# Kernel tuning notes

Measured on AMD Instinct MI355X. Metric: run time of the kernel, lower is better.

The kernel has to match this reference:

```python
import jax, jax.numpy as jnp
import numpy as np

B, T, IN_DIM = 16, 4096, 64
LAYER_DIM, OUT_DIM, NUM_LAYERS = 256, 64, 10


def _k1(w, b, x):
    # pointwise (kernel_size=1) conv: w [O,I], x [B,I,T] -> [B,O,T]
    return jnp.einsum('oi,bit->bot', w, x) + b[:, None]


def setup_inputs() -> dict:
    key = jax.random.key(0)
    ks = jax.random.split(key, 20)
    s = 0.05
    L = LAYER_DIM
    inp = {
        'x': jax.random.normal(ks[0], (B, T, IN_DIM), jnp.float32),
        'emb_w': jax.random.normal(ks[1], (L, IN_DIM), jnp.float32) * s,
        'emb_b': jax.random.normal(ks[2], (L,), jnp.float32) * s,
        'filt_w': jax.random.normal(ks[3], (NUM_LAYERS, L, L, 2), jnp.float32) * s,
        'filt_b': jax.random.normal(ks[4], (NUM_LAYERS, L), jnp.float32) * s,
        'gate_w': jax.random.normal(ks[5], (NUM_LAYERS, L, L, 2), jnp.float32) * s,
        'gate_b': jax.random.normal(ks[6], (NUM_LAYERS, L), jnp.float32) * s,
        'res_w': jax.random.normal(ks[7], (NUM_LAYERS, L, L), jnp.float32) * s,
        'res_b': jax.random.normal(ks[8], (NUM_LAYERS, L), jnp.float32) * s,
        'skip_w': jax.random.normal(ks[9], (NUM_LAYERS + 1, L, L), jnp.float32) * s,
        'skip_b': jax.random.normal(ks[10], (NUM_LAYERS + 1, L), jnp.float32) * s,
        'fin1_w': jax.random.normal(ks[11], (L, L), jnp.float32) * s,
        'fin1_b': jax.random.normal(ks[12], (L,), jnp.float32) * s,
        'fin2_w': jax.random.normal(ks[13], (L, L), jnp.float32) * s,
        'fin2_b': jax.random.normal(ks[14], (L,), jnp.float32) * s,
        'out_w': jax.random.normal(ks[15], (OUT_DIM, L), jnp.float32) * s,
        'out_b': jax.random.normal(ks[16], (OUT_DIM,), jnp.float32) * s,
    }
    return inp


def reference(x, emb_w, emb_b, filt_w, filt_b, gate_w, gate_b,
              res_w, res_b, skip_w, skip_b,
              fin1_w, fin1_b, fin2_w, fin2_b, out_w, out_b):
    # x: [B, T, IN] -> [B, IN, T]
    h = jnp.transpose(x, (0, 2, 1))
    h = jax.nn.relu(_k1(emb_w, emb_b, h))  # [B, L, T]
    final = _k1(skip_w[0], skip_b[0], h)
    Tlen = h.shape[-1]
    for i in range(NUM_LAYERS):
        dilate = 2 ** i
        # causal dilated conv, k=2: y[t] = W[...,1] @ h[t] + W[...,0] @ h[t-dilate]
        h_shift = jnp.pad(h, ((0, 0), (0, 0), (dilate, 0)))[:, :, :Tlen]
        def dconv(w, b):
            return (jnp.einsum('oi,bit->bot', w[:, :, 1], h) +
                    jnp.einsum('oi,bit->bot', w[:, :, 0], h_shift) + b[:, None])
        t_x = jnp.tanh(dconv(filt_w[i], filt_b[i]))
        s_x = jax.nn.sigmoid(dconv(gate_w[i], gate_b[i]))
        residual_x = _k1(res_w[i], res_b[i], h)
        gated = t_x * s_x
        skip_x = _k1(skip_w[i + 1], skip_b[i + 1], gated)
        h = skip_x + residual_x  # note: original code adds skip_x (not gated) to residual
        final = final + skip_x
    final = _k1(fin1_w, fin1_b, jax.nn.relu(final))
    final = _k1(fin2_w, fin2_b, jax.nn.relu(final))
    final = jnp.transpose(final, (0, 2, 1))  # [B, T, L]
    outputs = jnp.tanh(final @ out_w.T + out_b)  # apply_tanh=True
    return outputs
```

## Files before the change

kernel.cpp:

```cpp
#include <hip/hip_runtime.h>
#include <hip/hip_bf16.h>

#define Bn 16
#define Tn 4096
#define IN_DIM 64
#define L 256
#define NL 10
#define PADROWS 512
#define TP (Tn + PADROWS)
#define COLS 64

typedef __attribute__((ext_vector_type(8))) short short8;
typedef __attribute__((ext_vector_type(4))) float f32x4;
typedef unsigned short ushort_t;
typedef unsigned int uint_t;

__device__ inline ushort_t f2bf(float f) {
    uint_t u = __builtin_bit_cast(uint_t, f);
    u = u + 0x7fffu + ((u >> 16) & 1u);
    return (ushort_t)(u >> 16);
}

__device__ inline float fexp2f(float x) { return __builtin_amdgcn_exp2f(x); }
__device__ inline float frcpf(float x)  { return __builtin_amdgcn_rcpf(x); }
__device__ inline float tanh_fast(float x) {
    float e = fexp2f(x * 2.8853900817779268f);
    return 1.f - 2.f * frcpf(e + 1.f);
}
__device__ inline float sigm_fast(float x) {
    return frcpf(1.f + fexp2f(-1.4426950408889634f * x));
}

__device__ inline f32x4 mfma16(short8 a, short8 b, f32x4 c) {
    return __builtin_amdgcn_mfma_f32_16x16x32_bf16(a, b, c, 0, 0, 0);
}

__device__ inline void gld_lds16(const void* src, void* dst) {
    __builtin_amdgcn_global_load_lds(
        (const __attribute__((address_space(1))) void*)src,
        (__attribute__((address_space(3))) void*)dst, 16, 0, 0);
}

__device__ inline int xcd_swz(int bid) {
    return (bid & 7) * 128 + (bid >> 3);
}

__global__ void prep_kernel(
    const float* __restrict__ filt_w, const float* __restrict__ gate_w,
    const float* __restrict__ res_w,  const float* __restrict__ skip_w,
    const float* __restrict__ emb_w,  const float* __restrict__ fin1_w,
    const float* __restrict__ fin2_w, const float* __restrict__ out_w,
    ushort_t* __restrict__ Wfp, ushort_t* __restrict__ Wgp,
    ushort_t* __restrict__ Wrp, ushort_t* __restrict__ Wsp,
    ushort_t* __restrict__ Ws0, ushort_t* __restrict__ We,
    ushort_t* __restrict__ W1,  ushort_t* __restrict__ W2,
    ushort_t* __restrict__ Wo,
    ushort_t* __restrict__ h_a, ushort_t* __restrict__ h_b)
{
    const int stride = gridDim.x * blockDim.x;
    const int tid0 = blockIdx.x * blockDim.x + threadIdx.x;

    for (int idx = tid0; idx < NL * 16 * 1024 * 8; idx += stride) {
        int e  = idx & 7;
        int r  = (idx >> 3) & 15;
        int qq = (idx >> 7) & 3;
        int rg = (idx >> 9) & 15;
        int t  = (idx >> 13) & 15;
        int i  = idx >> 17;
        int row = rg * 16 + r;
        int k = t * 32 + qq * 8 + e;
        int tap = (k < 256) ? 1 : 0;
        int kk = k & 255;
        int src = ((i * 256 + row) * 256 + kk) * 2 + tap;
        Wfp[idx] = f2bf(filt_w[src]);
        Wgp[idx] = f2bf(gate_w[src]);
    }
    for (int idx = tid0; idx < NL * 8 * 1024 * 8; idx += stride) {
        int e  = idx & 7;
        int r  = (idx >> 3) & 15;
        int qq = (idx >> 7) & 3;
        int rg = (idx >> 9) & 15;
        int t  = (idx >> 13) & 7;
        int i  = idx >> 16;
        int row = rg * 16 + r;
        int k = t * 32 + qq * 8 + e;
        Wrp[idx] = f2bf(res_w[(i * 256 + row) * 256 + k]);
        Wsp[idx] = f2bf(skip_w[((i + 1) * 256 + row) * 256 + k]);
    }
    for (int idx = tid0; idx < L * L; idx += stride) {
        Ws0[idx] = f2bf(skip_w[idx]);
        W1[idx] = f2bf(fin1_w[idx]);
        W2[idx] = f2bf(fin2_w[idx]);
    }
    for (int idx = tid0; idx < L * IN_DIM; idx += stride) We[idx] = f2bf(emb_w[idx]);
    for (int idx = tid0; idx < 64 * L; idx += stride)     Wo[idx] = f2bf(out_w[idx]);
    for (int idx = tid0; idx < Bn * PADROWS * L; idx += stride) {
        int bb = idx >> 17;
        int r = idx & 131071;
        size_t off = (size_t)bb * TP * L + r;
        h_a[off] = 0;
        h_b[off] = 0;
    }
}

__global__ __launch_bounds__(512, 4) void emb_kernel(
    const float* __restrict__ x,
    const ushort_t* __restrict__ We, const float* __restrict__ eb,
    const ushort_t* __restrict__ Ws0, const float* __restrict__ sb0,
    ushort_t* __restrict__ h_out, float* __restrict__ fin)
{
    __shared__ __align__(16) char gt[32 * 1024];

    const int tid = threadIdx.x;
    const int w = tid >> 6;
    const int ln = tid & 63;
    const int q = ln >> 4;
    const int n16 = ln & 15;
    const int lid = xcd_swz(blockIdx.x);
    const int b = lid >> 6;
    const int t0 = (lid & 63) * COLS;
    const int row0 = w * 32;

    f32x4 acc[2][4];
    #pragma unroll
    for (int rt = 0; rt < 2; ++rt)
        #pragma unroll
        for (int ct = 0; ct < 4; ++ct) acc[rt][ct] = (f32x4){0.f, 0.f, 0.f, 0.f};

    #pragma unroll
    for (int ks = 0; ks < 2; ++ks) {
        const int k = ks * 32 + q * 8;
        short8 bfr[4];
        #pragma unroll
        for (int ct = 0; ct < 4; ++ct) {
            int c = ct * 16 + n16;
            const float* xp = x + ((size_t)(b * Tn + t0 + c)) * IN_DIM + k;
            f32x4 x0 = *(const f32x4*)xp;
            f32x4 x1 = *(const f32x4*)(xp + 4);
            short8 v;
            v[0] = (short)f2bf(x0[0]); v[1] = (short)f2bf(x0[1]);
            v[2] = (short)f2bf(x0[2]); v[3] = (short)f2bf(x0[3]);
            v[4] = (short)f2bf(x1[0]); v[5] = (short)f2bf(x1[1]);
            v[6] = (short)f2bf(x1[2]); v[7] = (short)f2bf(x1[3]);
            bfr[ct] = v;
        }
        #pragma unroll
        for (int rt = 0; rt < 2; ++rt) {
            int row = row0 + rt * 16 + n16;
            short8 a = *(const short8*)(We + row * IN_DIM + k);
            #pragma unroll
            for (int ct = 0; ct < 4; ++ct)
                acc[rt][ct] = mfma16(a, bfr[ct], acc[rt][ct]);
        }
    }

    ushort_t* hob = h_out + ((size_t)(b * TP + PADROWS + t0)) * L;
    #pragma unroll
    for (int rt = 0; rt < 2; ++rt) {
        int i0 = row0 + rt * 16 + q * 4;
        f32x4 eb4 = *(const f32x4*)(eb + i0);
        #pragma unroll
        for (int ct = 0; ct < 4; ++ct) {
            int c = ct * 16 + n16;
            f32x4 h0 = acc[rt][ct] + eb4;
            float v0 = fmaxf(h0[0], 0.f), v1 = fmaxf(h0[1], 0.f);
            float v2 = fmaxf(h0[2], 0.f), v3 = fmaxf(h0[3], 0.f);
            uint_t lo = (uint_t)f2bf(v0) | ((uint_t)f2bf(v1) << 16);
            uint_t hi = (uint_t)f2bf(v2) | ((uint_t)f2bf(v3) << 16);
            *(uint2*)(hob + (size_t)c * L + i0) = make_uint2(lo, hi);
            int byt = c * 512 + ((i0 * 2) ^ ((c & 7) << 4));
            *(uint2*)(gt + byt) = make_uint2(lo, hi);
        }
    }
    __syncthreads();

    f32x4 accs[2][4];
    #pragma unroll
    for (int rt = 0; rt < 2; ++rt)
        #pragma unroll
        for (int ct = 0; ct < 4; ++ct) accs[rt][ct] = (f32x4){0.f, 0.f, 0.f, 0.f};

    for (int ks = 0; ks < 8; ++ks) {
        const int k = ks * 32 + q * 8;
        short8 bg[4];
        #pragma unroll
        for (int ct = 0; ct < 4; ++ct) {
            int c = ct * 16 + n16;
            bg[ct] = *(const short8*)(gt + c * 512 + ((k * 2) ^ ((c & 7) << 4)));
        }
        #pragma unroll
        for (int rt = 0; rt < 2; ++rt) {
            int row = row0 + rt * 16 + n16;
            short8 a = *(const short8*)(Ws0 + row * L + k);
            #pragma unroll
            for (int ct = 0; ct < 4; ++ct)
                accs[rt][ct] = mfma16(a, bg[ct], accs[rt][ct]);
        }
    }
    float* fob = fin + ((size_t)(b * Tn + t0)) * L;
    #pragma unroll
    for (int rt = 0; rt < 2; ++rt) {
        int i0 = row0 + rt * 16 + q * 4;
        f32x4 sb4 = *(const f32x4*)(sb0 + i0);
        #pragma unroll
        for (int ct = 0; ct < 4; ++ct) {
            int c = ct * 16 + n16;
            *(f32x4*)(fob + (size_t)c * L + i0) = accs[rt][ct] + sb4;
        }
    }
}

__global__ __launch_bounds__(512, 4) void layer_kernel(
    const ushort_t* __restrict__ h_in, ushort_t* __restrict__ h_out,
    float* __restrict__ fin,
    const char* __restrict__ WfL, const char* __restrict__ WgL,
    const char* __restrict__ WrL, const char* __restrict__ WsL,
    const float* __restrict__ fb_, const float* __restrict__ gb_,
    const float* __restrict__ rb_, const float* __restrict__ sb_,
    int d)
{
    __shared__ __align__(16) char hh[64 * 1024];

    const int tid = threadIdx.x;
    const int w = tid >> 6;
    const int ln = tid & 63;
    const int q = ln >> 4;
    const int n16 = ln & 15;
    const int lid = xcd_swz(blockIdx.x);
    const int b = lid >> 6;
    const int t0 = (lid & 63) * COLS;

    const ushort_t* hbase = h_in + ((size_t)(b * TP + PADROWS + t0)) * L;
    #pragma unroll
    for (int it = 0; it < 8; ++it) {
        int c = it * 8 + w;
        int chunk = ln ^ (c & 7);
        int sh = (chunk >= 32) ? d : 0;
        const ushort_t* src = hbase + ((long)c - sh) * L + (chunk & 31) * 8;
        gld_lds16(src, hh + c * 1024);
    }
    __syncthreads();

    const char* pf = WfL + (w * 2) * 1024 + ln * 16;
    const char* pg = WgL + (w * 2) * 1024 + ln * 16;
    const char* ps = WsL + (w * 2) * 1024 + ln * 16;
    const char* pr = WrL + (w * 2) * 1024 + ln * 16;

    f32x4 accf[2][4], accg[2][4];
    #pragma unroll
    for (int rt = 0; rt < 2; ++rt)
        #pragma unroll
        for (int ct = 0; ct < 4; ++ct) {
            accf[rt][ct] = (f32x4){0.f, 0.f, 0.f, 0.f};
            accg[rt][ct] = (f32x4){0.f, 0.f, 0.f, 0.f};
        }

    short8 wf0 = *(const short8*)(pf);
    short8 wf1 = *(const short8*)(pf + 1024);
    short8 wg0 = *(const short8*)(pg);
    short8 wg1 = *(const short8*)(pg + 1024);
    for (int st = 0; st < 16; ++st) {
        const int nb = ((st < 15) ? st + 1 : 15) * 16384;
        short8 nf0 = *(const short8*)(pf + nb);
        short8 nf1 = *(const short8*)(pf + nb + 1024);
        short8 ng0 = *(const short8*)(pg + nb);
        short8 ng1 = *(const short8*)(pg + nb + 1024);
        const int kq2 = st * 64 + q * 16;
        #pragma unroll
        for (int ct = 0; ct < 4; ++ct) {
            int c = ct * 16 + n16;
            short8 bfr = *(const short8*)(hh + c * 1024 + (kq2 ^ ((c & 7) << 4)));
            accf[0][ct] = mfma16(wf0, bfr, accf[0][ct]);
            accf[1][ct] = mfma16(wf1, bfr, accf[1][ct]);
            accg[0][ct] = mfma16(wg0, bfr, accg[0][ct]);
            accg[1][ct] = mfma16(wg1, bfr, accg[1][ct]);
        }
        wf0 = nf0; wf1 = nf1; wg0 = ng0; wg1 = ng1;
    }
    __syncthreads();

    const int row0 = w * 32;
    #pragma unroll
    for (int rt = 0; rt < 2; ++rt) {
        int i0 = row0 + rt * 16 + q * 4;
        f32x4 fb4 = *(const f32x4*)(fb_ + i0);
        f32x4 gb4 = *(const f32x4*)(gb_ + i0);
        #pragma unroll
        for (int ct = 0; ct < 4; ++ct) {
            int c = ct * 16 + n16;
            uint_t pk[2];
            #pragma unroll
            for (int h2 = 0; h2 < 2; ++h2) {
                float v0 = tanh_fast(accf[rt][ct][h2 * 2] + fb4[h2 * 2]) *
                           sigm_fast(accg[rt][ct][h2 * 2] + gb4[h2 * 2]);
                float v1 = tanh_fast(accf[rt][ct][h2 * 2 + 1] + fb4[h2 * 2 + 1]) *
                           sigm_fast(accg[rt][ct][h2 * 2 + 1] + gb4[h2 * 2 + 1]);
                pk[h2] = (uint_t)f2bf(v0) | ((uint_t)f2bf(v1) << 16);
            }
            int byt = c * 1024 + ((512 + i0 * 2) ^ ((c & 7) << 4));
            *(uint2*)(hh + byt) = make_uint2(pk[0], pk[1]);
        }
    }
    __syncthreads();

    f32x4 accs[2][4], accr[2][4];
    #pragma unroll
    for (int rt = 0; rt < 2; ++rt)
        #pragma unroll
        for (int ct = 0; ct < 4; ++ct) {
            accs[rt][ct] = (f32x4){0.f, 0.f, 0.f, 0.f};
            accr[rt][ct] = (f32x4){0.f, 0.f, 0.f, 0.f};
        }

    short8 ws0 = *(const short8*)(ps);
    short8 ws1 = *(const short8*)(ps + 1024);
    short8 wr0 = *(const short8*)(pr);
    short8 wr1 = *(const short8*)(pr + 1024);
    for (int st = 0; st < 8; ++st) {
        const int nb = ((st < 7) ? st + 1 : 7) * 16384;
        short8 ns0 = *(const short8*)(ps + nb);
        short8 ns1 = *(const short8*)(ps + nb + 1024);
        short8 nr0 = *(const short8*)(pr + nb);
        short8 nr1 = *(const short8*)(pr + nb + 1024);
        const int kq2 = st * 64 + q * 16;
        #pragma unroll
        for (int ct = 0; ct < 4; ++ct) {
            int c = ct * 16 + n16;
            short8 bg = *(const short8*)(hh + c * 1024 +
                                         ((512 + kq2) ^ ((c & 7) << 4)));
            short8 bh = *(const short8*)(hh + c * 1024 + (kq2 ^ ((c & 7) << 4)));
            accs[0][ct] = mfma16(ws0, bg, accs[0][ct]);
            accs[1][ct] = mfma16(ws1, bg, accs[1][ct]);
            accr[0][ct] = mfma16(wr0, bh, accr[0][ct]);
            accr[1][ct] = mfma16(wr1, bh, accr[1][ct]);
        }
        ws0 = ns0; ws1 = ns1; wr0 = nr0; wr1 = nr1;
    }

    ushort_t* hob = h_out + ((size_t)(b * TP + PADROWS + t0)) * L;
    float* fob = fin + ((size_t)(b * Tn + t0)) * L;
    #pragma unroll
    for (int rt = 0; rt < 2; ++rt) {
        int i0 = row0 + rt * 16 + q * 4;
        f32x4 sb4 = *(const f32x4*)(sb_ + i0);
        f32x4 rb4 = *(const f32x4*)(rb_ + i0);
        #pragma unroll
        for (int ct = 0; ct < 4; ++ct) {
            int c = ct * 16 + n16;
            f32x4 sk = accs[rt][ct] + sb4;
            f32x4 hn = sk + accr[rt][ct] + rb4;
            uint_t lo = (uint_t)f2bf(hn[0]) | ((uint_t)f2bf(hn[1]) << 16);
            uint_t hi = (uint_t)f2bf(hn[2]) | ((uint_t)f2bf(hn[3]) << 16);
            *(uint2*)(hob + (size_t)c * L + i0) = make_uint2(lo, hi);
            f32x4* fp = (f32x4*)(fob + (size_t)c * L + i0);
            *fp = *fp + sk;
        }
    }
}

__global__ __launch_bounds__(512, 4) void final_kernel(
    const float* __restrict__ fin,
    const ushort_t* __restrict__ W1, const float* __restrict__ b1,
    const ushort_t* __restrict__ W2, const float* __restrict__ b2,
    const ushort_t* __restrict__ Wo, const float* __restrict__ ob,
    float* __restrict__ out)
{
    __shared__ __align__(16) char s1[32 * 1024];
    __shared__ __align__(16) char s2[32 * 1024];

    const int tid = threadIdx.x;
    const int w = tid >> 6;
    const int ln = tid & 63;
    const int q = ln >> 4;
    const int n16 = ln & 15;
    const int lid = xcd_swz(blockIdx.x);
    const int b = lid >> 6;
    const int t0 = (lid & 63) * COLS;
    const int row0 = w * 32;

    {
        int c = tid & 63;
        int kg = tid >> 6;
        const float* fp = fin + ((size_t)(b * Tn + t0 + c)) * L + kg * 32;
        #pragma unroll
        for (int j = 0; j < 8; ++j) {
            f32x4 v = *(const f32x4*)(fp + j * 4);
            uint_t lo = (uint_t)f2bf(fmaxf(v[0], 0.f)) | ((uint_t)f2bf(fmaxf(v[1], 0.f)) << 16);
            uint_t hi = (uint_t)f2bf(fmaxf(v[2], 0.f)) | ((uint_t)f2bf(fmaxf(v[3], 0.f)) << 16);
            int kk = kg * 32 + j * 4;
            *(uint2*)(s1 + c * 512 + ((kk * 2) ^ ((c & 7) << 4))) = make_uint2(lo, hi);
        }
    }
    __syncthreads();

    f32x4 acc[2][4];
    #pragma unroll
    for (int rt = 0; rt < 2; ++rt)
        #pragma unroll
        for (int ct = 0; ct < 4; ++ct) acc[rt][ct] = (f32x4){0.f, 0.f, 0.f, 0.f};
    for (int ks = 0; ks < 8; ++ks) {
        const int k = ks * 32 + q * 8;
        short8 bfr[4];
        #pragma unroll
        for (int ct = 0; ct < 4; ++ct) {
            int c = ct * 16 + n16;
            bfr[ct] = *(const short8*)(s1 + c * 512 + ((k * 2) ^ ((c & 7) << 4)));
        }
        #pragma unroll
        for (int rt = 0; rt < 2; ++rt) {
            int row = row0 + rt * 16 + n16;
            short8 a = *(const short8*)(W1 + row * L + k);
            #pragma unroll
            for (int ct = 0; ct < 4; ++ct) acc[rt][ct] = mfma16(a, bfr[ct], acc[rt][ct]);
        }
    }
    #pragma unroll
    for (int rt = 0; rt < 2; ++rt) {
        int i0 = row0 + rt * 16 + q * 4;
        f32x4 bb = *(const f32x4*)(b1 + i0);
        #pragma unroll
        for (int ct = 0; ct < 4; ++ct) {
            int c = ct * 16 + n16;
            f32x4 z = acc[rt][ct] + bb;
            uint_t lo = (uint_t)f2bf(fmaxf(z[0], 0.f)) | ((uint_t)f2bf(fmaxf(z[1], 0.f)) << 16);
            uint_t hi = (uint_t)f2bf(fmaxf(z[2], 0.f)) | ((uint_t)f2bf(fmaxf(z[3], 0.f)) << 16);
            *(uint2*)(s2 + c * 512 + ((i0 * 2) ^ ((c & 7) << 4))) = make_uint2(lo, hi);
        }
    }
    __syncthreads();

    #pragma unroll
    for (int rt = 0; rt < 2; ++rt)
        #pragma unroll
        for (int ct = 0; ct < 4; ++ct) acc[rt][ct] = (f32x4){0.f, 0.f, 0.f, 0.f};
    for (int ks = 0; ks < 8; ++ks) {
        const int k = ks * 32 + q * 8;
        short8 bfr[4];
        #pragma unroll
        for (int ct = 0; ct < 4; ++ct) {
            int c = ct * 16 + n16;
            bfr[ct] = *(const short8*)(s2 + c * 512 + ((k * 2) ^ ((c & 7) << 4)));
        }
        #pragma unroll
        for (int rt = 0; rt < 2; ++rt) {
            int row = row0 + rt * 16 + n16;
            short8 a = *(const short8*)(W2 + row * L + k);
            #pragma unroll
            for (int ct = 0; ct < 4; ++ct) acc[rt][ct] = mfma16(a, bfr[ct], acc[rt][ct]);
        }
    }
    #pragma unroll
    for (int rt = 0; rt < 2; ++rt) {
        int i0 = row0 + rt * 16 + q * 4;
        f32x4 bb = *(const f32x4*)(b2 + i0);
        #pragma unroll
        for (int ct = 0; ct < 4; ++ct) {
            int c = ct * 16 + n16;
            f32x4 z = acc[rt][ct] + bb;
            uint_t lo = (uint_t)f2bf(z[0]) | ((uint_t)f2bf(z[1]) << 16);
            uint_t hi = (uint_t)f2bf(z[2]) | ((uint_t)f2bf(z[3]) << 16);
            *(uint2*)(s1 + c * 512 + ((i0 * 2) ^ ((c & 7) << 4))) = make_uint2(lo, hi);
        }
    }
    __syncthreads();

    if (w < 4) {
        f32x4 acc3[4];
        #pragma unroll
        for (int ct = 0; ct < 4; ++ct) acc3[ct] = (f32x4){0.f, 0.f, 0.f, 0.f};
        for (int ks = 0; ks < 8; ++ks) {
            const int k = ks * 32 + q * 8;
            short8 bfr[4];
            #pragma unroll
            for (int ct = 0; ct < 4; ++ct) {
                int c = ct * 16 + n16;
                bfr[ct] = *(const short8*)(s1 + c * 512 + ((k * 2) ^ ((c & 7) << 4)));
            }
            short8 a = *(const short8*)(Wo + (w * 16 + n16) * L + k);
            #pragma unroll
            for (int ct = 0; ct < 4; ++ct) acc3[ct] = mfma16(a, bfr[ct], acc3[ct]);
        }
        int o0 = w * 16 + q * 4;
        f32x4 ob4 = *(const f32x4*)(ob + o0);
        float* obase = out + ((size_t)(b * Tn + t0)) * 64;
        #pragma unroll
        for (int ct = 0; ct < 4; ++ct) {
            int c = ct * 16 + n16;
            f32x4 v;
            #pragma unroll
            for (int j = 0; j < 4; ++j) v[j] = tanh_fast(acc3[ct][j] + ob4[j]);
            *(f32x4*)(obase + (size_t)c * 64 + o0) = v;
        }
    }
}

extern "C" void kernel_launch(void* const* d_in, const int* in_sizes, int n_in,
                              void* d_out, int out_size, void* d_ws, size_t ws_size,
                              hipStream_t stream)
{
    (void)in_sizes; (void)n_in; (void)out_size; (void)ws_size;
    const float* x      = (const float*)d_in[0];
    const float* emb_w  = (const float*)d_in[1];
    const float* emb_b  = (const float*)d_in[2];
    const float* filt_w = (const float*)d_in[3];
    const float* filt_b = (const float*)d_in[4];
    const float* gate_w = (const float*)d_in[5];
    const float* gate_b = (const float*)d_in[6];
    const float* res_w  = (const float*)d_in[7];
    const float* res_b  = (const float*)d_in[8];
    const float* skip_w = (const float*)d_in[9];
    const float* skip_b = (const float*)d_in[10];
    const float* fin1_w = (const float*)d_in[11];
    const float* fin1_b = (const float*)d_in[12];
    const float* fin2_w = (const float*)d_in[13];
    const float* fin2_b = (const float*)d_in[14];
    const float* out_w  = (const float*)d_in[15];
    const float* out_b  = (const float*)d_in[16];

    char* ws = (char*)d_ws;
    size_t off = 0;
    auto alloc = [&](size_t bytes) -> char* {
        char* p = ws + off;
        off += (bytes + 255) & ~(size_t)255;
        return p;
    };
    ushort_t* h_a = (ushort_t*)alloc((size_t)Bn * TP * L * 2);
    ushort_t* h_b = (ushort_t*)alloc((size_t)Bn * TP * L * 2);
    float*    fin = (float*)   alloc((size_t)Bn * Tn * L * 4);
    ushort_t* Wfp = (ushort_t*)alloc((size_t)NL * 16 * 1024 * 8 * 2);
    ushort_t* Wgp = (ushort_t*)alloc((size_t)NL * 16 * 1024 * 8 * 2);
    ushort_t* Wrp = (ushort_t*)alloc((size_t)NL * 8 * 1024 * 8 * 2);
    ushort_t* Wsp = (ushort_t*)alloc((size_t)NL * 8 * 1024 * 8 * 2);
    ushort_t* Ws0 = (ushort_t*)alloc((size_t)L * L * 2);
    ushort_t* We  = (ushort_t*)alloc((size_t)L * IN_DIM * 2);
    ushort_t* W1  = (ushort_t*)alloc((size_t)L * L * 2);
    ushort_t* W2  = (ushort_t*)alloc((size_t)L * L * 2);
    ushort_t* Wo  = (ushort_t*)alloc((size_t)64 * L * 2);

    prep_kernel<<<512, 256, 0, stream>>>(filt_w, gate_w, res_w, skip_w, emb_w,
        fin1_w, fin2_w, out_w, Wfp, Wgp, Wrp, Wsp, Ws0, We, W1, W2, Wo, h_a, h_b);

    emb_kernel<<<1024, 512, 0, stream>>>(x, We, emb_b, Ws0, skip_b, h_a, fin);

    ushort_t* hin = h_a;
    ushort_t* hout = h_b;
    for (int i = 0; i < NL; ++i) {
        layer_kernel<<<1024, 512, 0, stream>>>(hin, hout, fin,
            (const char*)Wfp + (size_t)i * 16 * 16384,
            (const char*)Wgp + (size_t)i * 16 * 16384,
            (const char*)Wrp + (size_t)i * 8 * 16384,
            (const char*)Wsp + (size_t)i * 8 * 16384,
            filt_b + i * L, gate_b + i * L, res_b + i * L, skip_b + (i + 1) * L,
            1 << i);
        ushort_t* t = hin; hin = hout; hout = t;
    }

    final_kernel<<<1024, 512, 0, stream>>>(fin, W1, fin1_b, W2, fin2_b,
        Wo, out_b, (float*)d_out);
}
```

Measured before the change: 1.027 ms.

## Store per-layer skip outputs as bf16 slabs and sum them in final kernel

Instead of each layer doing a read-modify-write on an fp32 skip accumulator (8 bytes of traffic per element per layer), each layer writes its skip output as bf16 into its own slab, and the final kernel reads all 11 slabs and sums them. Layer outputs are staged through LDS so the global stores are coalesced. A fallback path that coalesces the fp32 accumulation is kept for when the workspace is too small. The slab path needs much more workspace, and rounding skip values to bf16 before summing adds error.

```diff
diff --git a/kernel.cpp b/kernel.cpp
--- a/kernel.cpp
+++ b/kernel.cpp
@@ -19,6 +19,10 @@
     uint_t u = __builtin_bit_cast(uint_t, f);
     u = u + 0x7fffu + ((u >> 16) & 1u);
     return (ushort_t)(u >> 16);
+}
+__device__ inline float bf2f(ushort_t v) {
+    uint_t u = ((uint_t)v) << 16;
+    return __builtin_bit_cast(float, u);
 }
 
 __device__ inline float fexp2f(float x) { return __builtin_amdgcn_exp2f(x); }
@@ -103,11 +107,13 @@
     }
 }
 
+template<bool SLAB>
 __global__ __launch_bounds__(512, 4) void emb_kernel(
     const float* __restrict__ x,
     const ushort_t* __restrict__ We, const float* __restrict__ eb,
     const ushort_t* __restrict__ Ws0, const float* __restrict__ sb0,
-    ushort_t* __restrict__ h_out, float* __restrict__ fin)
+    ushort_t* __restrict__ h_out, ushort_t* __restrict__ skip0,
+    float* __restrict__ fin)
 {
     __shared__ __align__(16) char gt[32 * 1024];
 
@@ -197,7 +203,6 @@
                 accs[rt][ct] = mfma16(a, bg[ct], accs[rt][ct]);
         }
     }
-    float* fob = fin + ((size_t)(b * Tn + t0)) * L;
     #pragma unroll
     for (int rt = 0; rt < 2; ++rt) {
         int i0 = row0 + rt * 16 + q * 4;
@@ -205,14 +210,24 @@
         #pragma unroll
         for (int ct = 0; ct < 4; ++ct) {
             int c = ct * 16 + n16;
-            *(f32x4*)(fob + (size_t)c * L + i0) = accs[rt][ct] + sb4;
-        }
-    }
-}
-
+            f32x4 z = accs[rt][ct] + sb4;
+            if constexpr (SLAB) {
+                ushort_t* sob = skip0 + ((size_t)(b * Tn + t0)) * L;
+                uint_t lo = (uint_t)f2bf(z[0]) | ((uint_t)f2bf(z[1]) << 16);
+                uint_t hi = (uint_t)f2bf(z[2]) | ((uint_t)f2bf(z[3]) << 16);
+                *(uint2*)(sob + (size_t)c * L + i0) = make_uint2(lo, hi);
+            } else {
+                float* fob = fin + ((size_t)(b * Tn + t0)) * L;
+                *(f32x4*)(fob + (size_t)c * L + i0) = z;
+            }
+        }
+    }
+}
+
+template<bool SLAB>
 __global__ __launch_bounds__(512, 4) void layer_kernel(
     const ushort_t* __restrict__ h_in, ushort_t* __restrict__ h_out,
-    float* __restrict__ fin,
+    ushort_t* __restrict__ skip_out, float* __restrict__ fin,
     const char* __restrict__ WfL, const char* __restrict__ WgL,
     const char* __restrict__ WrL, const char* __restrict__ WsL,
     const float* __restrict__ fb_, const float* __restrict__ gb_,
@@ -297,7 +312,7 @@
                            sigm_fast(accg[rt][ct][h2 * 2 + 1] + gb4[h2 * 2 + 1]);
                 pk[h2] = (uint_t)f2bf(v0) | ((uint_t)f2bf(v1) << 16);
             }
-            int byt = c * 1024 + ((512 + i0 * 2) ^ ((c & 7) << 4));
+            int byt = c * 1024 + 512 + ((i0 * 2) ^ ((c & 7) << 4));
             *(uint2*)(hh + byt) = make_uint2(pk[0], pk[1]);
         }
     }
@@ -326,8 +341,8 @@
         #pragma unroll
         for (int ct = 0; ct < 4; ++ct) {
             int c = ct * 16 + n16;
-            short8 bg = *(const short8*)(hh + c * 1024 +
-                                         ((512 + kq2) ^ ((c & 7) << 4)));
+            short8 bg = *(const short8*)(hh + c * 1024 + 512 +
+                                         (kq2 ^ ((c & 7) << 4)));
             short8 bh = *(const short8*)(hh + c * 1024 + (kq2 ^ ((c & 7) << 4)));
             accs[0][ct] = mfma16(ws0, bg, accs[0][ct]);
             accs[1][ct] = mfma16(ws1, bg, accs[1][ct]);
@@ -336,9 +351,8 @@
         }
         ws0 = ns0; ws1 = ns1; wr0 = nr0; wr1 = nr1;
     }
-
-    ushort_t* hob = h_out + ((size_t)(b * TP + PADROWS + t0)) * L;
-    float* fob = fin + ((size_t)(b * Tn + t0)) * L;
+    __syncthreads();
+
     #pragma unroll
     for (int rt = 0; rt < 2; ++rt) {
         int i0 = row0 + rt * 16 + q * 4;
@@ -349,16 +363,44 @@
             int c = ct * 16 + n16;
             f32x4 sk = accs[rt][ct] + sb4;
             f32x4 hn = sk + accr[rt][ct] + rb4;
-            uint_t lo = (uint_t)f2bf(hn[0]) | ((uint_t)f2bf(hn[1]) << 16);
-            uint_t hi = (uint_t)f2bf(hn[2]) | ((uint_t)f2bf(hn[3]) << 16);
-            *(uint2*)(hob + (size_t)c * L + i0) = make_uint2(lo, hi);
-            f32x4* fp = (f32x4*)(fob + (size_t)c * L + i0);
-            *fp = *fp + sk;
-        }
-    }
-}
-
+            uint_t hlo = (uint_t)f2bf(hn[0]) | ((uint_t)f2bf(hn[1]) << 16);
+            uint_t hhi = (uint_t)f2bf(hn[2]) | ((uint_t)f2bf(hn[3]) << 16);
+            uint_t slo = (uint_t)f2bf(sk[0]) | ((uint_t)f2bf(sk[1]) << 16);
+            uint_t shi = (uint_t)f2bf(sk[2]) | ((uint_t)f2bf(sk[3]) << 16);
+            int sw = (i0 * 2) ^ ((c & 7) << 4);
+            *(uint2*)(hh + c * 1024 + sw) = make_uint2(hlo, hhi);
+            *(uint2*)(hh + c * 1024 + 512 + sw) = make_uint2(slo, shi);
+        }
+    }
+    __syncthreads();
+
+    ushort_t* hob = h_out + ((size_t)(b * TP + PADROWS + t0)) * L;
+    #pragma unroll
+    for (int it = 0; it < 8; ++it) {
+        int c = it * 8 + w;
+        short8 v = *(const short8*)(hh + c * 1024 + ((ln * 16) ^ ((c & 7) << 4)));
+        if constexpr (SLAB) {
+            ushort_t* sob = skip_out + ((size_t)(b * Tn + t0)) * L;
+            if (ln < 32) *(short8*)(hob + (size_t)c * L + ln * 8) = v;
+            else         *(short8*)(sob + (size_t)c * L + (ln - 32) * 8) = v;
+        } else {
+            if (ln < 32) *(short8*)(hob + (size_t)c * L + ln * 8) = v;
+            uint2 skb = *(const uint2*)(hh + c * 1024 + 512 +
+                                        ((ln * 8) ^ ((c & 7) << 4)));
+            float* fp = fin + ((size_t)(b * Tn + t0 + c)) * L + ln * 4;
+            f32x4 f = *(const f32x4*)fp;
+            f[0] += bf2f((ushort_t)(skb.x & 0xffff));
+            f[1] += bf2f((ushort_t)(skb.x >> 16));
+            f[2] += bf2f((ushort_t)(skb.y & 0xffff));
+            f[3] += bf2f((ushort_t)(skb.y >> 16));
+            *(f32x4*)fp = f;
+        }
+    }
+}
+
+template<bool SLAB>
 __global__ __launch_bounds__(512, 4) void final_kernel(
+    const ushort_t* __restrict__ skipbase, size_t slab,
     const float* __restrict__ fin,
     const ushort_t* __restrict__ W1, const float* __restrict__ b1,
     const ushort_t* __restrict__ W2, const float* __restrict__ b2,
@@ -378,7 +420,35 @@
     const int t0 = (lid & 63) * COLS;
     const int row0 = w * 32;
 
-    {
+    if constexpr (SLAB) {
+        const int c = tid >> 3;
+        const int j0 = tid & 7;
+        const size_t rowoff = ((size_t)(b * Tn + t0 + c)) * L;
+        float acc[4][8];
+        #pragma unroll
+        for (int jj = 0; jj < 4; ++jj)
+            #pragma unroll
+            for (int e = 0; e < 8; ++e) acc[jj][e] = 0.f;
+        for (int l = 0; l < NL + 1; ++l) {
+            const ushort_t* sp = skipbase + (size_t)l * slab + rowoff;
+            #pragma unroll
+            for (int jj = 0; jj < 4; ++jj) {
+                short8 v = *(const short8*)(sp + j0 * 8 + jj * 64);
+                #pragma unroll
+                for (int e = 0; e < 8; ++e)
+                    acc[jj][e] += bf2f((ushort_t)v[e]);
+            }
+        }
+        #pragma unroll
+        for (int jj = 0; jj < 4; ++jj) {
+            short8 v;
+            #pragma unroll
+            for (int e = 0; e < 8; ++e)
+                v[e] = (short)f2bf(fmaxf(acc[jj][e], 0.f));
+            int j = j0 + jj * 8;
+            *(short8*)(s1 + c * 512 + ((j * 16) ^ ((c & 7) << 4))) = v;
+        }
+    } else {
         int c = tid & 63;
         int kg = tid >> 6;
         const float* fp = fin + ((size_t)(b * Tn + t0 + c)) * L + kg * 32;
@@ -498,7 +568,7 @@
                               void* d_out, int out_size, void* d_ws, size_t ws_size,
                               hipStream_t stream)
 {
-    (void)in_sizes; (void)n_in; (void)out_size; (void)ws_size;
+    (void)in_sizes; (void)n_in; (void)out_size;
     const float* x      = (const float*)d_in[0];
     const float* emb_w  = (const float*)d_in[1];
     const float* emb_b  = (const float*)d_in[2];
@@ -517,6 +587,17 @@
     const float* out_w  = (const float*)d_in[15];
     const float* out_b  = (const float*)d_in[16];
 
+    const size_t SLAB = (size_t)Bn * Tn * L;
+    const size_t sz_h     = (size_t)Bn * TP * L * 2;
+    const size_t sz_slabs = (size_t)(NL + 1) * SLAB * 2;
+    const size_t sz_fin   = (size_t)Bn * Tn * L * 4;
+    const size_t sz_wfg   = (size_t)NL * 16 * 1024 * 8 * 2;
+    const size_t sz_wrs   = (size_t)NL * 8 * 1024 * 8 * 2;
+    const size_t sz_small = 3 * (size_t)L * L * 2 + (size_t)L * IN_DIM * 2 +
+                            (size_t)64 * L * 2 + 4096;
+    const size_t reqA = 2 * sz_h + sz_slabs + 2 * sz_wfg + 2 * sz_wrs + sz_small;
+    const bool useSlab = (ws_size >= reqA);
+
     char* ws = (char*)d_ws;
     size_t off = 0;
     auto alloc = [&](size_t bytes) -> char* {
@@ -524,13 +605,16 @@
         off += (bytes + 255) & ~(size_t)255;
         return p;
     };
-    ushort_t* h_a = (ushort_t*)alloc((size_t)Bn * TP * L * 2);
-    ushort_t* h_b = (ushort_t*)alloc((size_t)Bn * TP * L * 2);
-    float*    fin = (float*)   alloc((size_t)Bn * Tn * L * 4);
-    ushort_t* Wfp = (ushort_t*)alloc((size_t)NL * 16 * 1024 * 8 * 2);
-    ushort_t* Wgp = (ushort_t*)alloc((size_t)NL * 16 * 1024 * 8 * 2);
-    ushort_t* Wrp = (ushort_t*)alloc((size_t)NL * 8 * 1024 * 8 * 2);
-    ushort_t* Wsp = (ushort_t*)alloc((size_t)NL * 8 * 1024 * 8 * 2);
+    ushort_t* h_a   = (ushort_t*)alloc(sz_h);
+    ushort_t* h_b   = (ushort_t*)alloc(sz_h);
+    ushort_t* skipb = nullptr;
+    float*    fin   = nullptr;
+    if (useSlab) skipb = (ushort_t*)alloc(sz_slabs);
+    else         fin   = (float*)alloc(sz_fin);
+    ushort_t* Wfp = (ushort_t*)alloc(sz_wfg);
+    ushort_t* Wgp = (ushort_t*)alloc(sz_wfg);
+    ushort_t* Wrp = (ushort_t*)alloc(sz_wrs);
+    ushort_t* Wsp = (ushort_t*)alloc(sz_wrs);
     ushort_t* Ws0 = (ushort_t*)alloc((size_t)L * L * 2);
     ushort_t* We  = (ushort_t*)alloc((size_t)L * IN_DIM * 2);
     ushort_t* W1  = (ushort_t*)alloc((size_t)L * L * 2);
@@ -540,21 +624,41 @@
     prep_kernel<<<512, 256, 0, stream>>>(filt_w, gate_w, res_w, skip_w, emb_w,
         fin1_w, fin2_w, out_w, Wfp, Wgp, Wrp, Wsp, Ws0, We, W1, W2, Wo, h_a, h_b);
 
-    emb_kernel<<<1024, 512, 0, stream>>>(x, We, emb_b, Ws0, skip_b, h_a, fin);
-
-    ushort_t* hin = h_a;
-    ushort_t* hout = h_b;
-    for (int i = 0; i < NL; ++i) {
-        layer_kernel<<<1024, 512, 0, stream>>>(hin, hout, fin,
-            (const char*)Wfp + (size_t)i * 16 * 16384,
-            (const char*)Wgp + (size_t)i * 16 * 16384,
-            (const char*)Wrp + (size_t)i * 8 * 16384,
-            (const char*)Wsp + (size_t)i * 8 * 16384,
-            filt_b + i * L, gate_b + i * L, res_b + i * L, skip_b + (i + 1) * L,
-            1 << i);
-        ushort_t* t = hin; hin = hout; hout = t;
-    }
-
-    final_kernel<<<1024, 512, 0, stream>>>(fin, W1, fin1_b, W2, fin2_b,
-        Wo, out_b, (float*)d_out);
-}
+    if (useSlab) {
+        emb_kernel<true><<<1024, 512, 0, stream>>>(x, We, emb_b, Ws0, skip_b,
+            h_a, skipb, nullptr);
+        ushort_t* hin = h_a;
+        ushort_t* hout = h_b;
+        for (int i = 0; i < NL; ++i) {
+            layer_kernel<true><<<1024, 512, 0, stream>>>(hin, hout,
+                skipb + (size_t)(i + 1) * SLAB, nullptr,
+                (const char*)Wfp + (size_t)i * 16 * 16384,
+                (const char*)Wgp + (size_t)i * 16 * 16384,
+                (const char*)Wrp + (size_t)i * 8 * 16384,
+                (const char*)Wsp + (size_t)i * 8 * 16384,
+                filt_b + i * L, gate_b + i * L, res_b + i * L,
+                skip_b + (i + 1) * L, 1 << i);
+            ushort_t* t = hin; hin = hout; hout = t;
+        }
+        final_kernel<true><<<1024, 512, 0, stream>>>(skipb, SLAB, nullptr,
+            W1, fin1_b, W2, fin2_b, Wo, out_b, (float*)d_out);
+    } else {
+        emb_kernel<false><<<1024, 512, 0, stream>>>(x, We, emb_b, Ws0, skip_b,
+            h_a, nullptr, fin);
+        ushort_t* hin = h_a;
+        ushort_t* hout = h_b;
+        for (int i = 0; i < NL; ++i) {
+            layer_kernel<false><<<1024, 512, 0, stream>>>(hin, hout,
+                nullptr, fin,
+                (const char*)Wfp + (size_t)i * 16 * 16384,
+                (const char*)Wgp + (size_t)i * 16 * 16384,
+                (const char*)Wrp + (size_t)i * 8 * 16384,
+                (const char*)Wsp + (size_t)i * 8 * 16384,
+                filt_b + i * L, gate_b + i * L, res_b + i * L,
+                skip_b + (i + 1) * L, 1 << i);
+            ushort_t* t = hin; hin = hout; hout = t;
+        }
+        final_kernel<false><<<1024, 512, 0, stream>>>(nullptr, SLAB, fin,
+            W1, fin1_b, W2, fin2_b, Wo, out_b, (float*)d_out);
+    }
+}
```

Measured after the change: 965.3 us. 1.06x faster.
